# Optimization experiments

Hardware: AMD Instinct MI355X
Metric: run time of the kernel (lower is better)

## Reference

```python
import jax, jax.numpy as jnp
import numpy as np

KNN_K = 3
EPS = 1e-8


def _make_poses(key, batch):
    """Random valid SE(3) matrices [B,4,4] (rotation via QR, small translation)."""
    k1, k2 = jax.random.split(key)
    A = jax.random.normal(k1, (batch, 3, 3), dtype=jnp.float32)
    Q, _ = jnp.linalg.qr(A)
    det = jnp.linalg.det(Q)[:, None, None]
    Q = Q * jnp.where(det < 0, -1.0, 1.0)  # ensure proper rotation
    t = jax.random.normal(k2, (batch, 3), dtype=jnp.float32) * 0.5
    pose = jnp.tile(jnp.eye(4, dtype=jnp.float32), (batch, 1, 1))
    pose = pose.at[:, :3, :3].set(Q)
    pose = pose.at[:, :3, 3].set(t)
    return pose


def setup_inputs() -> dict:
    key = jax.random.key(0)
    kq, kr, kf, kp0, kp1 = jax.random.split(key, 5)
    B, N, M = 2, 8192, 8192
    pc0 = jax.random.normal(kq, (B, N, 3), dtype=jnp.float32) * 20.0
    pc1 = jax.random.normal(kr, (B, M, 3), dtype=jnp.float32) * 20.0
    flow1 = jax.random.normal(kf, (B, M, 3), dtype=jnp.float32)
    pose0 = _make_poses(kp0, B)
    pose1 = _make_poses(kp1, B)
    return {"pc0": pc0, "pc1": pc1, "flow1": flow1, "pose0": pose0, "pose1": pose1}


def reference(pc0, pc1, flow1, pose0, pose1):
    # cal_pose0to1: transform from pc0 ego frame into pc1 ego frame
    pose_0to1 = jnp.linalg.inv(pose1) @ pose0            # [B,4,4]
    R = pose_0to1[:, :3, :3]                             # [B,3,3]
    t = pose_0to1[:, :3, 3]                              # [B,3]
    # pc0_in_pc1 = pc0 @ R^T + t
    pc0_t = jnp.einsum("bij,bnj->bni", R, pc0) + t[:, None, :]  # [B,N,3]
    pose_flow = pc0_t - pc0                              # ego-motion displacement

    # pairwise squared distances (cdist^2) via GEMM form: [B,N,M]
    q2 = jnp.sum(pc0_t * pc0_t, axis=-1)                 # [B,N]
    r2 = jnp.sum(pc1 * pc1, axis=-1)                     # [B,M]
    cross = jnp.einsum("bnd,bmd->bnm", pc0_t, pc1)
    d2 = q2[:, :, None] + r2[:, None, :] - 2.0 * cross

    # KNN: k smallest distances
    neg_d2, idx = jax.lax.top_k(-d2, KNN_K)              # [B,N,k]
    d = jnp.sqrt(jnp.maximum(-neg_d2, 0.0))

    # inverse-distance weights over the k neighbors
    w = 1.0 / (d + EPS)
    w = w / jnp.sum(w, axis=-1, keepdims=True)           # [B,N,k]

    # gather neighbor flows: flow1 [B,M,3] -> [B,N,k,3]
    gathered = jnp.take_along_axis(flow1[:, None, :, :], idx[..., None], axis=2)
    flow_interp = jnp.sum(w[..., None] * gathered, axis=2)  # [B,N,3]
    return flow_interp, pose_flow
```

## Files before the change

### kernel.cpp

```cpp
#include <hip/hip_runtime.h>
#include <math.h>
#include <float.h>
#include <limits.h>

#define CS   128
#define CT   16
#define TILE_PTS (CT * CS)
#define CSP  129
#define QB1  32
#define QT   8
#define MARGIN 0.05f
typedef unsigned long long ull;
#define KMAX 0xFFFFFFFFFFFFFFFFull

__device__ __forceinline__ unsigned int ford(float f) {
    unsigned int b = __float_as_uint(f);
    return b ^ (((unsigned int)((int)b >> 31)) | 0x80000000u);
}
__device__ __forceinline__ float funord(unsigned int u) {
    unsigned int m = ((u >> 31) - 1u) | 0x80000000u;
    return __uint_as_float(u ^ m);
}

__device__ __forceinline__ ull umin64(ull a, ull b) { return a < b ? a : b; }
__device__ __forceinline__ ull umax64(ull a, ull b) { return a > b ? a : b; }

__device__ __forceinline__ void ins3k(ull k, ull& k0, ull& k1, ull& k2) {
    ull n2 = umax64(k1, umin64(k2, k));
    ull n1 = umax64(k0, umin64(k1, k));
    k0 = umin64(k0, k);
    k1 = n1;
    k2 = n2;
}

__device__ __forceinline__ ull wmin64(ull k) {
    #pragma unroll
    for (int m = 1; m <= 32; m <<= 1) {
        ull o = __shfl_xor(k, m);
        k = o < k ? o : k;
    }
    return k;
}
__device__ __forceinline__ float wminf(float v) {
    #pragma unroll
    for (int m = 1; m <= 32; m <<= 1)
        v = fminf(v, __shfl_xor(v, m));
    return v;
}

__device__ __forceinline__ void pose_rel(const float* __restrict__ P0,
                                         const float* __restrict__ P1,
                                         float R[3][3], float tv[3])
{
    float dt0 = P0[3]  - P1[3];
    float dt1 = P0[7]  - P1[7];
    float dt2 = P0[11] - P1[11];
    #pragma unroll
    for (int i = 0; i < 3; ++i) {
        float a0 = P1[i], a1 = P1[4 + i], a2 = P1[8 + i];
        #pragma unroll
        for (int j = 0; j < 3; ++j)
            R[i][j] = fmaf(a2, P0[8 + j], fmaf(a1, P0[4 + j], a0 * P0[j]));
        tv[i] = fmaf(a2, dt2, fmaf(a1, dt1, a0 * dt0));
    }
}

__launch_bounds__(256, 4)
__global__ void knn_phaseA(const float* __restrict__ pc0,
                           const float* __restrict__ pc1,
                           const float* __restrict__ pose0,
                           const float* __restrict__ pose1,
                           float* __restrict__ cmin,
                           int B, int N, int M, int cstride)
{
    __shared__ float4 tile[CT * CSP];
    __shared__ float4 qd[QB1];

    const int tid = threadIdx.x;
    const int b   = blockIdx.z;
    const int ctb = blockIdx.y;
    const int qb  = blockIdx.x * QB1;
    const int pbase = ctb * TILE_PTS;

    if (tid < QB1) {
        float R[3][3], tv[3];
        pose_rel(pose0 + b * 16, pose1 + b * 16, R, tv);
        int qg0 = qb + tid;
        int qg  = (qg0 < N) ? qg0 : (N - 1);
        const float px = pc0[(size_t)(b * N + qg) * 3 + 0];
        const float py = pc0[(size_t)(b * N + qg) * 3 + 1];
        const float pz = pc0[(size_t)(b * N + qg) * 3 + 2];
        float qx = fmaf(R[0][2], pz, fmaf(R[0][1], py, R[0][0] * px)) + tv[0];
        float qy = fmaf(R[1][2], pz, fmaf(R[1][1], py, R[1][0] * px)) + tv[1];
        float qz = fmaf(R[2][2], pz, fmaf(R[2][1], py, R[2][0] * px)) + tv[2];
        qd[tid] = make_float4(qx, qy, qz,
                              (qx * qx + qy * qy) + qz * qz);
    }

    #pragma unroll
    for (int k = 0; k < TILE_PTS / (256 * 4); ++k) {
        const int pl = (tid + k * 256) * 4;
        const int p  = pbase + pl;
        float4* dst = &tile[(pl >> 7) * CSP + (pl & (CS - 1))];
        if (p + 3 < M) {
            const float4* pf = (const float4*)(pc1 + (size_t)(b * M + p) * 3);
            float4 A = pf[0], Bv = pf[1], C = pf[2];
            dst[0] = make_float4(-2.f * A.x, -2.f * A.y, -2.f * A.z,
                                 (A.x * A.x + A.y * A.y) + A.z * A.z);
            dst[1] = make_float4(-2.f * A.w, -2.f * Bv.x, -2.f * Bv.y,
                                 (A.w * A.w + Bv.x * Bv.x) + Bv.y * Bv.y);
            dst[2] = make_float4(-2.f * Bv.z, -2.f * Bv.w, -2.f * C.x,
                                 (Bv.z * Bv.z + Bv.w * Bv.w) + C.x * C.x);
            dst[3] = make_float4(-2.f * C.y, -2.f * C.z, -2.f * C.w,
                                 (C.y * C.y + C.z * C.z) + C.w * C.w);
        } else {
            #pragma unroll
            for (int u = 0; u < 4; ++u) {
                int pp = p + u;
                float4 v;
                if (pp < M) {
                    const float* s = pc1 + (size_t)(b * M + pp) * 3;
                    float x = s[0], y = s[1], z = s[2];
                    v = make_float4(-2.f * x, -2.f * y, -2.f * z,
                                    (x * x + y * y) + z * z);
                } else {
                    v = make_float4(0.f, 0.f, 0.f, FLT_MAX);
                }
                dst[u] = v;
            }
        }
    }
    __syncthreads();

    const int w    = tid >> 6;
    const int lane = tid & 63;
    const int cl   = lane & 15;
    const int part = lane >> 4;

    float4 q0 = qd[w * QT + 0], q1 = qd[w * QT + 1];
    float4 q2 = qd[w * QT + 2], q3 = qd[w * QT + 3];
    float4 q4 = qd[w * QT + 4], q5 = qd[w * QT + 5];
    float4 q6 = qd[w * QT + 6], q7 = qd[w * QT + 7];

    float m0 = FLT_MAX, m1 = FLT_MAX, m2 = FLT_MAX, m3 = FLT_MAX;
    float m4 = FLT_MAX, m5 = FLT_MAX, m6 = FLT_MAX, m7 = FLT_MAX;

    const float4* tp = &tile[cl * CSP + part * 32];
    #pragma unroll 8
    for (int i = 0; i < 32; ++i) {
        const float4 v = tp[i];
        m0 = fminf(m0, fmaf(q0.x, v.x, fmaf(q0.y, v.y, fmaf(q0.z, v.z, v.w))));
        m1 = fminf(m1, fmaf(q1.x, v.x, fmaf(q1.y, v.y, fmaf(q1.z, v.z, v.w))));
        m2 = fminf(m2, fmaf(q2.x, v.x, fmaf(q2.y, v.y, fmaf(q2.z, v.z, v.w))));
        m3 = fminf(m3, fmaf(q3.x, v.x, fmaf(q3.y, v.y, fmaf(q3.z, v.z, v.w))));
        m4 = fminf(m4, fmaf(q4.x, v.x, fmaf(q4.y, v.y, fmaf(q4.z, v.z, v.w))));
        m5 = fminf(m5, fmaf(q5.x, v.x, fmaf(q5.y, v.y, fmaf(q5.z, v.z, v.w))));
        m6 = fminf(m6, fmaf(q6.x, v.x, fmaf(q6.y, v.y, fmaf(q6.z, v.z, v.w))));
        m7 = fminf(m7, fmaf(q7.x, v.x, fmaf(q7.y, v.y, fmaf(q7.z, v.z, v.w))));
    }

    #pragma unroll
    for (int msk = 16; msk <= 32; msk <<= 1) {
        m0 = fminf(m0, __shfl_xor(m0, msk));
        m1 = fminf(m1, __shfl_xor(m1, msk));
        m2 = fminf(m2, __shfl_xor(m2, msk));
        m3 = fminf(m3, __shfl_xor(m3, msk));
        m4 = fminf(m4, __shfl_xor(m4, msk));
        m5 = fminf(m5, __shfl_xor(m5, msk));
        m6 = fminf(m6, __shfl_xor(m6, msk));
        m7 = fminf(m7, __shfl_xor(m7, msk));
    }

    if (part == 0) {
        const int cg = ctb * CT + cl;
        float mv[QT] = {m0, m1, m2, m3, m4, m5, m6, m7};
        #pragma unroll
        for (int t = 0; t < QT; ++t) {
            int qg0 = qb + w * QT + t;
            int qg  = (qg0 < N) ? qg0 : (N - 1);
            cmin[((size_t)b * N + qg) * cstride + cg] = mv[t];
        }
    }
}

__launch_bounds__(256, 8)
__global__ void knn_select(const float* __restrict__ pc0,
                           const float* __restrict__ pc1,
                           const float* __restrict__ flow1,
                           const float* __restrict__ pose0,
                           const float* __restrict__ pose1,
                           const float* __restrict__ cmin,
                           float* __restrict__ out,
                           int B, int N, int M, int cstride)
{
    const int tid  = threadIdx.x;
    const int w    = tid >> 6;
    const int lane = tid & 63;
    const int b    = blockIdx.y;
    const int q    = blockIdx.x * 4 + w;
    if (q >= N) return;

    const int ncc = (M + CS - 1) / CS;
    float key = (lane < ncc) ? cmin[((size_t)b * N + q) * cstride + lane]
                             : FLT_MAX;

    float R[3][3], tv[3];
    pose_rel(pose0 + b * 16, pose1 + b * 16, R, tv);
    const float px = pc0[(size_t)(b * N + q) * 3 + 0];
    const float py = pc0[(size_t)(b * N + q) * 3 + 1];
    const float pz = pc0[(size_t)(b * N + q) * 3 + 2];
    const float qx = fmaf(R[0][2], pz, fmaf(R[0][1], py, R[0][0] * px)) + tv[0];
    const float qy = fmaf(R[1][2], pz, fmaf(R[1][1], py, R[1][0] * px)) + tv[1];
    const float qz = fmaf(R[2][2], pz, fmaf(R[2][1], py, R[2][0] * px)) + tv[2];
    const float q2 = (qx * qx + qy * qy) + qz * qz;

    if (lane == 0) {
        size_t pf = (size_t)B * N * 3 + (size_t)(b * N + q) * 3;
        out[pf + 0] = qx - px;
        out[pf + 1] = qy - py;
        out[pf + 2] = qz - pz;
    }

    float v = key;
    float t0 = wminf(v); v = (v == t0) ? FLT_MAX : v;
    float t1 = wminf(v); v = (v == t1) ? FLT_MAX : v;
    float t2 = wminf(v);
    const float thr = t2 + MARGIN;
    ull mask = __ballot(key <= thr);

    ull k0 = KMAX, k1 = KMAX, k2 = KMAX;
    while (mask) {
        const int ck = (int)__builtin_ctzll(mask);
        mask &= mask - 1;
        #pragma unroll
        for (int r = 0; r < CS / 64; ++r) {
            const int m = ck * CS + r * 64 + lane;
            if (m < M) {
                const float* pp = pc1 + (size_t)(b * M + m) * 3;
                float x = pp[0], y = pp[1], z = pp[2];
                float r2 = (x * x + y * y) + z * z;
                float cr = fmaf(qz, z, fmaf(qy, y, qx * x));
                float dd = fmaf(-2.0f, cr, q2 + r2);
                ull kk = ((ull)ford(dd) << 32) | (unsigned int)m;
                ins3k(kk, k0, k1, k2);
            }
        }
    }

    ull g0 = wmin64(k0);
    { bool e = (k0 == g0); k0 = e ? k1 : k0; k1 = e ? k2 : k1; }
    ull g1 = wmin64(k0);
    { bool e = (k0 == g1); k0 = e ? k1 : k0; }
    ull g2 = wmin64(k0);

    if (lane == 0) {
        float D0 = funord((unsigned int)(g0 >> 32));
        float D1 = funord((unsigned int)(g1 >> 32));
        float D2 = funord((unsigned int)(g2 >> 32));
        int   i0 = (int)(unsigned int)g0;
        int   i1 = (int)(unsigned int)g1;
        int   i2 = (int)(unsigned int)g2;

        float dd0 = sqrtf(fmaxf(D0, 0.f));
        float dd1 = sqrtf(fmaxf(D1, 0.f));
        float dd2 = sqrtf(fmaxf(D2, 0.f));
        float w0 = 1.0f / (dd0 + 1e-8f);
        float w1 = 1.0f / (dd1 + 1e-8f);
        float w2 = 1.0f / (dd2 + 1e-8f);
        float wsum = (w0 + w1) + w2;
        w0 /= wsum; w1 /= wsum; w2 /= wsum;

        const float* f0 = flow1 + (size_t)(b * M + i0) * 3;
        const float* f1 = flow1 + (size_t)(b * M + i1) * 3;
        const float* f2 = flow1 + (size_t)(b * M + i2) * 3;

        const size_t ob = (size_t)(b * N + q) * 3;
        #pragma unroll
        for (int c = 0; c < 3; ++c) {
            float p0 = w0 * f0[c];
            float p1 = w1 * f1[c];
            float p2 = w2 * f2[c];
            out[ob + c] = (p0 + p1) + p2;
        }
    }
}

extern "C" void kernel_launch(void* const* d_in, const int* in_sizes, int n_in,
                              void* d_out, int out_size, void* d_ws, size_t ws_size,
                              hipStream_t stream) {
    const float* pc0   = (const float*)d_in[0];
    const float* pc1   = (const float*)d_in[1];
    const float* flow1 = (const float*)d_in[2];
    const float* pose0 = (const float*)d_in[3];
    const float* pose1 = (const float*)d_in[4];
    float* out = (float*)d_out;

    const int B = in_sizes[3] / 16;
    const int N = in_sizes[0] / (3 * B);
    const int M = in_sizes[1] / (3 * B);

    const int nct     = (M + TILE_PTS - 1) / TILE_PTS;
    const int cstride = nct * CT;

    float* cmin = (float*)d_ws;

    dim3 g1((N + QB1 - 1) / QB1, nct, B);
    knn_phaseA<<<g1, dim3(256), 0, stream>>>(pc0, pc1, pose0, pose1,
                                             cmin, B, N, M, cstride);

    dim3 g2((N + 3) / 4, B);
    knn_select<<<g2, dim3(256), 0, stream>>>(pc0, pc1, flow1, pose0, pose1,
                                             cmin, out, B, N, M, cstride);
}
```

Measured before the change: 39.71 us.

## Process four queries per wavefront in KNN select and double phaseA query tile

Phase A now computes 16 queries per wave (64 per block), which halves the number of blocks and the repeated tile loads, at the cost of more registers per thread. The select kernel maps four queries onto each wavefront using 16-lane groups. Each group reads its candidate-chunk minima with float4 loads and keeps a running top-3 with med3 in place of repeated full-wave min reductions. Each lane now scans 8 points per candidate chunk instead of 2, split across two interleaved top-3 lists for more ILP, then merges them with butterfly shuffles. The intent is to cut the per-query shuffle and reduction cost and the idle lanes, at the price of longer serial scans per lane.

```diff
diff --git a/kernel.cpp b/kernel.cpp
--- a/kernel.cpp
+++ b/kernel.cpp
@@ -7,8 +7,8 @@
 #define CT   16
 #define TILE_PTS (CT * CS)
 #define CSP  129
-#define QB1  32
-#define QT   8
+#define QB1  64
+#define QT   16
 #define MARGIN 0.05f
 typedef unsigned long long ull;
 #define KMAX 0xFFFFFFFFFFFFFFFFull
@@ -33,19 +33,13 @@
     k2 = n2;
 }
 
-__device__ __forceinline__ ull wmin64(ull k) {
-    #pragma unroll
-    for (int m = 1; m <= 32; m <<= 1) {
-        ull o = __shfl_xor(k, m);
-        k = o < k ? o : k;
-    }
-    return k;
-}
-__device__ __forceinline__ float wminf(float v) {
-    #pragma unroll
-    for (int m = 1; m <= 32; m <<= 1)
-        v = fminf(v, __shfl_xor(v, m));
-    return v;
+__device__ __forceinline__ void sins(float d, float& a0, float& a1, float& a2)
+{
+    float n1 = __builtin_amdgcn_fmed3f(a0, a1, d);
+    float n2 = __builtin_amdgcn_fmed3f(a1, a2, d);
+    a0 = fminf(a0, d);
+    a1 = n1;
+    a2 = n2;
 }
 
 __device__ __forceinline__ void pose_rel(const float* __restrict__ P0,
@@ -137,48 +131,38 @@
     const int cl   = lane & 15;
     const int part = lane >> 4;
 
-    float4 q0 = qd[w * QT + 0], q1 = qd[w * QT + 1];
-    float4 q2 = qd[w * QT + 2], q3 = qd[w * QT + 3];
-    float4 q4 = qd[w * QT + 4], q5 = qd[w * QT + 5];
-    float4 q6 = qd[w * QT + 6], q7 = qd[w * QT + 7];
-
-    float m0 = FLT_MAX, m1 = FLT_MAX, m2 = FLT_MAX, m3 = FLT_MAX;
-    float m4 = FLT_MAX, m5 = FLT_MAX, m6 = FLT_MAX, m7 = FLT_MAX;
+    float4 qv[QT];
+    #pragma unroll
+    for (int t = 0; t < QT; ++t) qv[t] = qd[w * QT + t];
+
+    float mm[QT];
+    #pragma unroll
+    for (int t = 0; t < QT; ++t) mm[t] = FLT_MAX;
 
     const float4* tp = &tile[cl * CSP + part * 32];
-    #pragma unroll 8
+    #pragma unroll 4
     for (int i = 0; i < 32; ++i) {
         const float4 v = tp[i];
-        m0 = fminf(m0, fmaf(q0.x, v.x, fmaf(q0.y, v.y, fmaf(q0.z, v.z, v.w))));
-        m1 = fminf(m1, fmaf(q1.x, v.x, fmaf(q1.y, v.y, fmaf(q1.z, v.z, v.w))));
-        m2 = fminf(m2, fmaf(q2.x, v.x, fmaf(q2.y, v.y, fmaf(q2.z, v.z, v.w))));
-        m3 = fminf(m3, fmaf(q3.x, v.x, fmaf(q3.y, v.y, fmaf(q3.z, v.z, v.w))));
-        m4 = fminf(m4, fmaf(q4.x, v.x, fmaf(q4.y, v.y, fmaf(q4.z, v.z, v.w))));
-        m5 = fminf(m5, fmaf(q5.x, v.x, fmaf(q5.y, v.y, fmaf(q5.z, v.z, v.w))));
-        m6 = fminf(m6, fmaf(q6.x, v.x, fmaf(q6.y, v.y, fmaf(q6.z, v.z, v.w))));
-        m7 = fminf(m7, fmaf(q7.x, v.x, fmaf(q7.y, v.y, fmaf(q7.z, v.z, v.w))));
+        #pragma unroll
+        for (int t = 0; t < QT; ++t)
+            mm[t] = fminf(mm[t],
+                fmaf(qv[t].x, v.x, fmaf(qv[t].y, v.y, fmaf(qv[t].z, v.z, v.w))));
     }
 
     #pragma unroll
     for (int msk = 16; msk <= 32; msk <<= 1) {
-        m0 = fminf(m0, __shfl_xor(m0, msk));
-        m1 = fminf(m1, __shfl_xor(m1, msk));
-        m2 = fminf(m2, __shfl_xor(m2, msk));
-        m3 = fminf(m3, __shfl_xor(m3, msk));
-        m4 = fminf(m4, __shfl_xor(m4, msk));
-        m5 = fminf(m5, __shfl_xor(m5, msk));
-        m6 = fminf(m6, __shfl_xor(m6, msk));
-        m7 = fminf(m7, __shfl_xor(m7, msk));
+        #pragma unroll
+        for (int t = 0; t < QT; ++t)
+            mm[t] = fminf(mm[t], __shfl_xor(mm[t], msk));
     }
 
     if (part == 0) {
         const int cg = ctb * CT + cl;
-        float mv[QT] = {m0, m1, m2, m3, m4, m5, m6, m7};
         #pragma unroll
         for (int t = 0; t < QT; ++t) {
             int qg0 = qb + w * QT + t;
             int qg  = (qg0 < N) ? qg0 : (N - 1);
-            cmin[((size_t)b * N + qg) * cstride + cg] = mv[t];
+            cmin[((size_t)b * N + qg) * cstride + cg] = mm[t];
         }
     }
 }
@@ -196,13 +180,25 @@
     const int tid  = threadIdx.x;
     const int w    = tid >> 6;
     const int lane = tid & 63;
+    const int g    = lane >> 4;
+    const int l    = lane & 15;
     const int b    = blockIdx.y;
-    const int q    = blockIdx.x * 4 + w;
-    if (q >= N) return;
-
-    const int ncc = (M + CS - 1) / CS;
-    float key = (lane < ncc) ? cmin[((size_t)b * N + q) * cstride + lane]
-                             : FLT_MAX;
+    const int q0   = blockIdx.x * 16 + w * 4 + g;
+    const bool qvalid = (q0 < N);
+    const int q    = qvalid ? q0 : (N - 1);
+
+    const int ncc = cstride;
+    const size_t row = (size_t)(b * N + q) * cstride;
+    float c0, c1, c2, c3;
+    if (l * 4 + 3 < ncc) {
+        float4 cv = *(const float4*)&cmin[row + l * 4];
+        c0 = cv.x; c1 = cv.y; c2 = cv.z; c3 = cv.w;
+    } else {
+        c0 = (l * 4 + 0 < ncc) ? cmin[row + l * 4 + 0] : FLT_MAX;
+        c1 = (l * 4 + 1 < ncc) ? cmin[row + l * 4 + 1] : FLT_MAX;
+        c2 = (l * 4 + 2 < ncc) ? cmin[row + l * 4 + 2] : FLT_MAX;
+        c3 = (l * 4 + 3 < ncc) ? cmin[row + l * 4 + 3] : FLT_MAX;
+    }
 
     float R[3][3], tv[3];
     pose_rel(pose0 + b * 16, pose1 + b * 16, R, tv);
@@ -214,27 +210,38 @@
     const float qz = fmaf(R[2][2], pz, fmaf(R[2][1], py, R[2][0] * px)) + tv[2];
     const float q2 = (qx * qx + qy * qy) + qz * qz;
 
-    if (lane == 0) {
-        size_t pf = (size_t)B * N * 3 + (size_t)(b * N + q) * 3;
-        out[pf + 0] = qx - px;
-        out[pf + 1] = qy - py;
-        out[pf + 2] = qz - pz;
-    }
-
-    float v = key;
-    float t0 = wminf(v); v = (v == t0) ? FLT_MAX : v;
-    float t1 = wminf(v); v = (v == t1) ? FLT_MAX : v;
-    float t2 = wminf(v);
-    const float thr = t2 + MARGIN;
-    ull mask = __ballot(key <= thr);
-
-    ull k0 = KMAX, k1 = KMAX, k2 = KMAX;
+    float a0 = FLT_MAX, a1 = FLT_MAX, a2 = FLT_MAX;
+    sins(c0, a0, a1, a2);
+    sins(c1, a0, a1, a2);
+    sins(c2, a0, a1, a2);
+    sins(c3, a0, a1, a2);
+    #pragma unroll
+    for (int msk = 1; msk <= 8; msk <<= 1) {
+        float o0 = __shfl_xor(a0, msk);
+        float o1 = __shfl_xor(a1, msk);
+        float o2 = __shfl_xor(a2, msk);
+        sins(o0, a0, a1, a2);
+        sins(o1, a0, a1, a2);
+        sins(o2, a0, a1, a2);
+    }
+    const float thr = a2 + MARGIN;
+
+    ull mask = ((ull)(c0 <= thr) << (4 * l + 0))
+             | ((ull)(c1 <= thr) << (4 * l + 1))
+             | ((ull)(c2 <= thr) << (4 * l + 2))
+             | ((ull)(c3 <= thr) << (4 * l + 3));
+    #pragma unroll
+    for (int msk = 1; msk <= 8; msk <<= 1)
+        mask |= __shfl_xor(mask, msk);
+
+    ull kA0 = KMAX, kA1 = KMAX, kA2 = KMAX;
+    ull kB0 = KMAX, kB1 = KMAX, kB2 = KMAX;
     while (mask) {
         const int ck = (int)__builtin_ctzll(mask);
         mask &= mask - 1;
         #pragma unroll
-        for (int r = 0; r < CS / 64; ++r) {
-            const int m = ck * CS + r * 64 + lane;
+        for (int r = 0; r < CS / 16; ++r) {
+            const int m = ck * CS + r * 16 + l;
             if (m < M) {
                 const float* pp = pc1 + (size_t)(b * M + m) * 3;
                 float x = pp[0], y = pp[1], z = pp[2];
@@ -242,24 +249,37 @@
                 float cr = fmaf(qz, z, fmaf(qy, y, qx * x));
                 float dd = fmaf(-2.0f, cr, q2 + r2);
                 ull kk = ((ull)ford(dd) << 32) | (unsigned int)m;
-                ins3k(kk, k0, k1, k2);
+                if (r & 1) ins3k(kk, kB0, kB1, kB2);
+                else       ins3k(kk, kA0, kA1, kA2);
             }
         }
     }
-
-    ull g0 = wmin64(k0);
-    { bool e = (k0 == g0); k0 = e ? k1 : k0; k1 = e ? k2 : k1; }
-    ull g1 = wmin64(k0);
-    { bool e = (k0 == g1); k0 = e ? k1 : k0; }
-    ull g2 = wmin64(k0);
-
-    if (lane == 0) {
-        float D0 = funord((unsigned int)(g0 >> 32));
-        float D1 = funord((unsigned int)(g1 >> 32));
-        float D2 = funord((unsigned int)(g2 >> 32));
-        int   i0 = (int)(unsigned int)g0;
-        int   i1 = (int)(unsigned int)g1;
-        int   i2 = (int)(unsigned int)g2;
+    ins3k(kB0, kA0, kA1, kA2);
+    ins3k(kB1, kA0, kA1, kA2);
+    ins3k(kB2, kA0, kA1, kA2);
+
+    #pragma unroll
+    for (int msk = 1; msk <= 8; msk <<= 1) {
+        ull o0 = __shfl_xor(kA0, msk);
+        ull o1 = __shfl_xor(kA1, msk);
+        ull o2 = __shfl_xor(kA2, msk);
+        ins3k(o0, kA0, kA1, kA2);
+        ins3k(o1, kA0, kA1, kA2);
+        ins3k(o2, kA0, kA1, kA2);
+    }
+
+    if (l == 0 && qvalid) {
+        size_t pf = (size_t)B * N * 3 + (size_t)(b * N + q) * 3;
+        out[pf + 0] = qx - px;
+        out[pf + 1] = qy - py;
+        out[pf + 2] = qz - pz;
+
+        float D0 = funord((unsigned int)(kA0 >> 32));
+        float D1 = funord((unsigned int)(kA1 >> 32));
+        float D2 = funord((unsigned int)(kA2 >> 32));
+        int   i0 = (int)(unsigned int)kA0;
+        int   i1 = (int)(unsigned int)kA1;
+        int   i2 = (int)(unsigned int)kA2;
 
         float dd0 = sqrtf(fmaxf(D0, 0.f));
         float dd1 = sqrtf(fmaxf(D1, 0.f));
@@ -308,7 +328,7 @@
     knn_phaseA<<<g1, dim3(256), 0, stream>>>(pc0, pc1, pose0, pose1,
                                              cmin, B, N, M, cstride);
 
-    dim3 g2((N + 3) / 4, B);
+    dim3 g2((N + 15) / 16, B);
     knn_select<<<g2, dim3(256), 0, stream>>>(pc0, pc1, flow1, pose0, pose1,
                                              cmin, out, B, N, M, cstride);
 }
```

After: 34.07 us. -14.2%, faster.
